# Kernel tuning notes

Measured on AMD Instinct MI355X. Metric: run time of the kernel, lower is better.

The kernel has to match this reference:

```python
import jax, jax.numpy as jnp
import numpy as np
from jax import lax

B, N, T_IN, F_IN = 64, 800, 15, 8
T_OUT = 12
H = 64
NC = 9
KS = [2, 2, 2, 3, 3, 3, 4, 4, 4]
DS = [1, 2, 4, 1, 2, 4, 1, 2, 4]


def setup_inputs() -> dict:
    key = jax.random.key(0)
    ks = jax.random.split(key, 16)
    s = 0.1
    f32 = jnp.float32
    inp = {}
    inp['A'] = jnp.zeros((1,), f32)  # deprecated graph arg, unused
    inp['X'] = jax.random.normal(ks[0], (B, N, T_IN, F_IN), f32)
    # dilated conv weights grouped by kernel size (comps 0-2 k=2, 3-5 k=3, 6-8 k=4)
    inp['convw2'] = jax.random.normal(ks[1], (3, F_IN, F_IN, 2), f32) * s
    inp['convw3'] = jax.random.normal(ks[2], (3, F_IN, F_IN, 3), f32) * s
    inp['convw4'] = jax.random.normal(ks[3], (3, F_IN, F_IN, 4), f32) * s
    inp['convb'] = jax.random.normal(ks[4], (NC, F_IN), f32) * s
    # encoder GRU params (PyTorch layout: W_ih (3H,F), W_hh (3H,H))
    inp['enc_wih'] = jax.random.normal(ks[5], (NC, 3 * H, F_IN), f32) * s
    inp['enc_whh'] = jax.random.normal(ks[6], (NC, 3 * H, H), f32) * s
    inp['enc_bih'] = jax.random.normal(ks[7], (NC, 3 * H), f32) * s
    inp['enc_bhh'] = jax.random.normal(ks[8], (NC, 3 * H), f32) * s
    # decoder GRUCell params (input size 1)
    inp['dec_wih'] = jax.random.normal(ks[9], (NC, 3 * H, 1), f32) * s
    inp['dec_whh'] = jax.random.normal(ks[10], (NC, 3 * H, H), f32) * s
    inp['dec_bih'] = jax.random.normal(ks[11], (NC, 3 * H), f32) * s
    inp['dec_bhh'] = jax.random.normal(ks[12], (NC, 3 * H), f32) * s
    # per-comp readout Linear(H, 1)
    inp['lin_w'] = jax.random.normal(ks[13], (NC, 1, H), f32) * s
    inp['lin_b'] = jax.random.normal(ks[14], (NC, 1), f32) * s
    # node-wise component mixing embedding
    inp['embed'] = jax.random.normal(ks[15], (N, NC), f32)
    return inp


def gru_cell(x, h, wih, whh, bih, bhh):
    # PyTorch GRU semantics
    gi = x @ wih.T + bih  # (B, 3H)
    gh = h @ whh.T + bhh  # (B, 3H)
    ir, iz, in_ = jnp.split(gi, 3, axis=-1)
    hr, hz, hn = jnp.split(gh, 3, axis=-1)
    r = jax.nn.sigmoid(ir + hr)
    z = jax.nn.sigmoid(iz + hz)
    n = jnp.tanh(in_ + r * hn)
    return (1.0 - z) * n + z * h


def reference(A, X, convw2, convw3, convw4, convb, enc_wih, enc_whh, enc_bih,
              enc_bhh, dec_wih, dec_whh, dec_bih, dec_bhh, lin_w, lin_b, embed):
    del A  # deprecated in pure TS model
    Xf = X.reshape(-1, T_IN, F_IN)            # (B*N, T, F)
    xt = jnp.transpose(Xf, (0, 2, 1))         # (B*N, F, T) for conv NCH
    last0 = Xf[:, -1, 0:1]                    # X1[-1, :, 0] -> (B*N, 1)
    BN = Xf.shape[0]
    conv_ws = [convw2[0], convw2[1], convw2[2], convw3[0], convw3[1],
               convw3[2], convw4[0], convw4[1], convw4[2]]
    outs = []
    for r in range(NC):
        # dilated conv over time, VALID padding (length shrinks by d*(k-1))
        h = lax.conv_general_dilated(xt, conv_ws[r], (1,), 'VALID',
                                     rhs_dilation=(DS[r],),
                                     dimension_numbers=('NCH', 'OIH', 'NCH'))
        h = h + convb[r][None, :, None]
        seq = jnp.transpose(h, (2, 0, 1))     # time-major (L, B*N, F)

        ewih, ewhh, ebih, ebhh = enc_wih[r], enc_whh[r], enc_bih[r], enc_bhh[r]

        def enc_step(hc, x_t):
            return gru_cell(x_t, hc, ewih, ewhh, ebih, ebhh), None

        h_enc, _ = lax.scan(enc_step, jnp.zeros((BN, H), X.dtype), seq)

        dwih, dwhh, dbih, dbhh = dec_wih[r], dec_whh[r], dec_bih[r], dec_bhh[r]
        lw, lb = lin_w[r], lin_b[r]

        def dec_step(carry, _):
            hd, lv = carry
            hd = gru_cell(lv, hd, dwih, dwhh, dbih, dbhh)
            v = hd @ lw.T + lb                # (B*N, 1)
            # torch code feeds value.detach() back in
            return (hd, lax.stop_gradient(v)), v[:, 0]

        _, vals = lax.scan(dec_step, (h_enc, last0), None, length=T_OUT)
        outs.append(jnp.transpose(vals).reshape(B, N, T_OUT))  # (B, N, T_out)
    out = jnp.stack(outs, axis=-1)            # (B, N, T_out, NC)
    w = jax.nn.softmax(embed, axis=-1)        # (N, NC)
    return jnp.einsum('bntc,nc->bnt', out, w)
```

## Files before the change

kernel.cpp:

```cpp
#include <hip/hip_runtime.h>
#include <hip/hip_bf16.h>
#include <stdint.h>

typedef unsigned short u16;
typedef unsigned int   u32;
typedef float f32x4  __attribute__((ext_vector_type(4)));
typedef short bf16x8 __attribute__((ext_vector_type(8)));

#define NSEQ 800
#define TOUT 12
#define NC   9
#define LOG2E  1.44269504088896340736f
#define LOG2E2 2.88539008177792681472f

#define BH_OFF 0
#define BX_OFF 24576
#define H_OFF  36864
#define LDS_TOTAL 53248

__device__ __forceinline__ u16 f2bf(float f){ union{float f;u32 i;}v; v.f=f; u32 x=v.i; return (u16)((x + 0x7fffu + ((x>>16)&1u))>>16); }
__device__ __forceinline__ u32 pkbf(float a, float b){
  union{ __hip_bfloat162 h2; u32 u; } v;
  v.h2 = __float22bfloat162_rn(float2{a,b});
  return v.u;
}

union BXU { uint4 u; bf16x8 v; };

__global__ __launch_bounds__(512, 2) void rnn_kernel(
  const float* __restrict__ X,
  const float* __restrict__ cw2, const float* __restrict__ cw3, const float* __restrict__ cw4,
  const float* __restrict__ cbv,
  const float* __restrict__ Ewih, const float* __restrict__ Ewhh,
  const float* __restrict__ Ebih, const float* __restrict__ Ebhh,
  const float* __restrict__ Dwih, const float* __restrict__ Dwhh,
  const float* __restrict__ Dbih, const float* __restrict__ Dbhh,
  const float* __restrict__ Lw,   const float* __restrict__ Lb,
  const float* __restrict__ emb,
  float* __restrict__ out)
{
  __shared__ char LDSC[LDS_TOTAL];
  const int tid = threadIdx.x;
  const int wv  = tid >> 6;
  const int l   = tid & 63;
  const int q   = l >> 4;
  const int n   = l & 15;
  const int r   = blockIdx.y;
  const int seqb = blockIdx.x*128 + wv*16;

  const int Kc[NC]={2,2,2,3,3,3,4,4,4};
  const int Dc[NC]={1,2,4,1,2,4,1,2,4};
  const int K = Kc[r], D = Dc[r];
  const int L = 15 - (K-1)*D;

  const int HB = H_OFF + wv*2048;
  *(uint4*)(LDSC + HB + l*32)      = uint4{0,0,0,0};
  *(uint4*)(LDSC + HB + l*32 + 16) = uint4{0,0,0,0};

  auto stage_Bh = [&](const float* __restrict__ whh){
    #pragma unroll 1
    for (int it=0; it<3; it++){
      int slot = it*512 + tid;
      int g = slot >> 6, fl = slot & 63;
      int ks = g/12, nt = g%12;
      int col = nt*16 + (fl&15);
      float s = (nt<8) ? LOG2E : LOG2E2;
      u32 w[4] = {0,0,0,0};
      #pragma unroll
      for (int j=0;j<8;j++){
        int hid = ((j&3)<<4) | (ks*8 + (fl>>4)*2 + (j>>2));
        w[j>>1] |= (u32)f2bf(s * whh[col*64 + hid]) << ((j&1)*16);
      }
      *(uint4*)(LDSC + BH_OFF + slot*16) = uint4{w[0],w[1],w[2],w[3]};
    }
  };
  auto stage_Bx_enc = [&](){
    const float* wih = Ewih + r*192*8;
    const float* cw  = (r<3) ? (cw2 + r*128) : (r<6) ? (cw3 + (r-3)*192) : (cw4 + (r-6)*256);
    #pragma unroll 1
    for (int it=0; it<2; it++){
      int slot = it*512 + tid;
      if (slot < 768){
        int g = slot >> 6, fl = slot & 63;
        int col = g*16 + (fl&15);
        int tap = fl>>4;
        float s = (g<8) ? LOG2E : LOG2E2;
        u32 w[4] = {0,0,0,0};
        if (tap < K){
          #pragma unroll
          for (int j=0;j<8;j++){
            float a = 0.f;
            #pragma unroll
            for (int o=0;o<8;o++) a += wih[col*8+o]*cw[(o*8+j)*K + tap];
            w[j>>1] |= (u32)f2bf(s*a) << ((j&1)*16);
          }
        }
        *(uint4*)(LDSC + BX_OFF + slot*16) = uint4{w[0],w[1],w[2],w[3]};
      }
    }
  };
  auto stage_Bx_dec = [&](){
    const float* dwih = Dwih + r*192;
    #pragma unroll 1
    for (int it=0; it<2; it++){
      int slot = it*512 + tid;
      if (slot < 768){
        int g = slot >> 6, fl = slot & 63;
        int col = g*16 + (fl&15);
        float s = (g<8) ? LOG2E : LOG2E2;
        u32 w0 = ((fl>>4)==0) ? (u32)f2bf(s*dwih[col]) : 0u;
        *(uint4*)(LDSC + BX_OFF + slot*16) = uint4{w0,0,0,0};
      }
    }
  };

  stage_Bh(Ewhh + (size_t)r*192*64);
  stage_Bx_enc();

  float bR4[4], bZ4[4], bNi4[4], bNh4[4];
  {
    const float* bi = Ebih + r*192; const float* bh2 = Ebhh + r*192;
    const float* wih = Ewih + r*192*8; const float* cb = cbv + r*8;
    #pragma unroll
    for (int ht=0; ht<4; ht++){
      int hid = ht*16 + n;
      float cR=0.f,cZ=0.f,cN=0.f;
      #pragma unroll
      for (int o=0;o<8;o++){
        cR += wih[hid*8+o]*cb[o];
        cZ += wih[(64+hid)*8+o]*cb[o];
        cN += wih[(128+hid)*8+o]*cb[o];
      }
      bR4[ht]  = LOG2E  * (bi[hid]     + bh2[hid]     + cR);
      bZ4[ht]  = LOG2E  * (bi[64+hid]  + bh2[64+hid]  + cZ);
      bNi4[ht] = LOG2E2 * (bi[128+hid]                + cN);
      bNh4[ht] = LOG2E2 *                bh2[128+hid];
    }
  }

  float hO[4][4];
  #pragma unroll
  for (int ht=0;ht<4;ht++) for (int i=0;i<4;i++) hO[ht][i]=0.f;

  const int ra0 = HB + n*128 + (((  q + n)&7)<<4);
  const int ra1 = HB + n*128 + (((4+q + n)&7)<<4);
  int wa[4];
  #pragma unroll
  for (int i=0;i<4;i++){
    int seq = q*4+i;
    wa[i] = HB + seq*128 + ((((n>>1) + seq)&7)<<4) + ((n&1)<<3);
  }

  auto step_core = [&](bf16x8 ax){
    bf16x8 a0 = *(const bf16x8*)(LDSC + ra0);
    bf16x8 a1 = *(const bf16x8*)(LDSC + ra1);
    float hsv[4]; u32 pk01[4], pk23[4];
    #pragma unroll
    for (int ht=0; ht<4; ht++){
      bf16x8 bR0 = *(const bf16x8*)(LDSC + BH_OFF + ((      ht)*64 + l)*16);
      bf16x8 bR1 = *(const bf16x8*)(LDSC + BH_OFF + ((12  + ht)*64 + l)*16);
      bf16x8 bZ0 = *(const bf16x8*)(LDSC + BH_OFF + (( 4 + ht)*64 + l)*16);
      bf16x8 bZ1 = *(const bf16x8*)(LDSC + BH_OFF + ((16  + ht)*64 + l)*16);
      bf16x8 bN0 = *(const bf16x8*)(LDSC + BH_OFF + (( 8 + ht)*64 + l)*16);
      bf16x8 bN1 = *(const bf16x8*)(LDSC + BH_OFF + ((20  + ht)*64 + l)*16);
      bf16x8 xR  = *(const bf16x8*)(LDSC + BX_OFF + ((      ht)*64 + l)*16);
      bf16x8 xZ  = *(const bf16x8*)(LDSC + BX_OFF + (( 4 + ht)*64 + l)*16);
      bf16x8 xN  = *(const bf16x8*)(LDSC + BX_OFF + (( 8 + ht)*64 + l)*16);
      f32x4 aR  = f32x4{bR4[ht],bR4[ht],bR4[ht],bR4[ht]};
      f32x4 aZ  = f32x4{bZ4[ht],bZ4[ht],bZ4[ht],bZ4[ht]};
      f32x4 aNi = f32x4{bNi4[ht],bNi4[ht],bNi4[ht],bNi4[ht]};
      f32x4 aNh = f32x4{bNh4[ht],bNh4[ht],bNh4[ht],bNh4[ht]};
      aR = __builtin_amdgcn_mfma_f32_16x16x32_bf16(a0, bR0, aR,0,0,0);
      aR = __builtin_amdgcn_mfma_f32_16x16x32_bf16(a1, bR1, aR,0,0,0);
      aR = __builtin_amdgcn_mfma_f32_16x16x32_bf16(ax, xR,  aR,0,0,0);
      aZ = __builtin_amdgcn_mfma_f32_16x16x32_bf16(a0, bZ0, aZ,0,0,0);
      aZ = __builtin_amdgcn_mfma_f32_16x16x32_bf16(a1, bZ1, aZ,0,0,0);
      aZ = __builtin_amdgcn_mfma_f32_16x16x32_bf16(ax, xZ,  aZ,0,0,0);
      aNh= __builtin_amdgcn_mfma_f32_16x16x32_bf16(a0, bN0, aNh,0,0,0);
      aNh= __builtin_amdgcn_mfma_f32_16x16x32_bf16(a1, bN1, aNh,0,0,0);
      aNi= __builtin_amdgcn_mfma_f32_16x16x32_bf16(ax, xN,  aNi,0,0,0);
      #pragma unroll
      for (int i=0;i<4;i++){
        float rr = __builtin_amdgcn_rcpf(1.f + __builtin_amdgcn_exp2f(-aR[i]));
        float zz = __builtin_amdgcn_rcpf(1.f + __builtin_amdgcn_exp2f(-aZ[i]));
        float y  = aNi[i] + rr*aNh[i];
        float nn = 1.f - 2.f*__builtin_amdgcn_rcpf(__builtin_amdgcn_exp2f(y) + 1.f);
        float hn = nn + zz*(hO[ht][i]-nn);
        hO[ht][i] = hn;
        if (ht==0)      hsv[i] = hn;
        else if (ht==1) pk01[i] = pkbf(hsv[i], hn);
        else if (ht==2) hsv[i] = hn;
        else            pk23[i] = pkbf(hsv[i], hn);
      }
    }
    #pragma unroll
    for (int i=0;i<4;i++){
      uint2 wv2; wv2.x = pk01[i]; wv2.y = pk23[i];
      *(uint2*)(LDSC + wa[i]) = wv2;
    }
  };

  const float* xb = X + (size_t)(seqb + n)*120 + ((q<K)? q:0)*D*8;
  float4 c0 = *(const float4*)(xb);
  float4 c1 = *(const float4*)(xb + 4);
  __syncthreads();
  #pragma unroll 1
  for (int t=0; t<L; t++){
    int tn = (t+1 < L) ? (t+1) : t;
    float4 n0 = *(const float4*)(xb + tn*8);
    float4 n1 = *(const float4*)(xb + tn*8 + 4);
    BXU a;
    a.u.x = __builtin_amdgcn_perm(__float_as_uint(c0.y), __float_as_uint(c0.x), 0x07060302u);
    a.u.y = __builtin_amdgcn_perm(__float_as_uint(c0.w), __float_as_uint(c0.z), 0x07060302u);
    a.u.z = __builtin_amdgcn_perm(__float_as_uint(c1.y), __float_as_uint(c1.x), 0x07060302u);
    a.u.w = __builtin_amdgcn_perm(__float_as_uint(c1.w), __float_as_uint(c1.z), 0x07060302u);
    step_core(a.v);
    c0 = n0; c1 = n1;
  }

  __syncthreads();
  stage_Bh(Dwhh + (size_t)r*192*64);
  stage_Bx_dec();
  {
    const float* bi = Dbih + r*192; const float* bh2 = Dbhh + r*192;
    #pragma unroll
    for (int ht=0; ht<4; ht++){
      int hid = ht*16 + n;
      bR4[ht]  = LOG2E  * (bi[hid]     + bh2[hid]);
      bZ4[ht]  = LOG2E  * (bi[64+hid]  + bh2[64+hid]);
      bNi4[ht] = LOG2E2 *  bi[128+hid];
      bNh4[ht] = LOG2E2 *  bh2[128+hid];
    }
  }
  float lwr[4];
  #pragma unroll
  for (int ht=0; ht<4; ht++) lwr[ht] = Lw[r*64 + ht*16 + n];
  const float lb_ = Lb[r];
  float wgt;
  {
    int nb = (seqb + n) % NSEQ;
    float e[NC], mx = -1e30f;
    #pragma unroll
    for (int c=0;c<NC;c++){ e[c] = emb[nb*NC+c]; mx = fmaxf(mx, e[c]); }
    float sm = 0.f;
    #pragma unroll
    for (int c=0;c<NC;c++) sm += __expf(e[c]-mx);
    wgt = __expf(e[r]-mx) / sm;
  }
  float lv = X[(size_t)(seqb + n)*120 + 112];
  __syncthreads();

  #pragma unroll 1
  for (int t=0; t<TOUT; t++){
    BXU a; a.u = uint4{0,0,0,0};
    if (q==0) a.u.x = (u32)f2bf(lv);
    step_core(a.v);
    float p[4];
    #pragma unroll
    for (int i=0;i<4;i++)
      p[i] = hO[0][i]*lwr[0] + hO[1][i]*lwr[1] + hO[2][i]*lwr[2] + hO[3][i]*lwr[3];
    #pragma unroll
    for (int m=1; m<16; m<<=1){
      #pragma unroll
      for (int i=0;i<4;i++) p[i] += __shfl_xor(p[i], m, 64);
    }
    float s0 = (n&2) ? p[2] : p[0];
    float s1 = (n&2) ? p[3] : p[1];
    float se = (n&1) ? s1 : s0;
    float v = __shfl(se, (n>>2)*16 + (n&3), 64) + lb_;
    lv = v;
    if (q==0) atomicAdd(out + (size_t)(seqb+n)*TOUT + t, wgt*v);
  }
}

extern "C" void kernel_launch(void* const* d_in, const int* in_sizes, int n_in,
                              void* d_out, int out_size, void* d_ws, size_t ws_size,
                              hipStream_t stream)
{
  float* out = (float*)d_out;
  hipMemsetAsync(out, 0, (size_t)out_size*sizeof(float), stream);

  dim3 g(NSEQ*64/128, NC);
  rnn_kernel<<<g, 512, 0, stream>>>(
    (const float*)d_in[1],
    (const float*)d_in[2], (const float*)d_in[3], (const float*)d_in[4],
    (const float*)d_in[5],
    (const float*)d_in[6], (const float*)d_in[7], (const float*)d_in[8], (const float*)d_in[9],
    (const float*)d_in[10],(const float*)d_in[11],(const float*)d_in[12],(const float*)d_in[13],
    (const float*)d_in[14],(const float*)d_in[15],
    (const float*)d_in[16],
    out);
}
```

Before: 924.1 us.

## Keep GRU hidden state in registers by transposing MFMA operand roles

Swaps the MFMA A/B operands so the weights act as the row operand and the hidden state as the column operand. The new hidden state then stays in each lane's registers in the layout the next step's MFMA needs. This removes the per-step LDS write/read round trip of the hidden state and its swizzle, and shrinks LDS usage. The weight staging permutation and bias vectors are re-laid out to match, and the readout reduction becomes a per-lane dot product plus two cross-lane shuffles. Launch bounds drop to one block per SIMD pair hint, which may change register allocation and occupancy.

```diff
diff --git a/kernel.cpp b/kernel.cpp
--- a/kernel.cpp
+++ b/kernel.cpp
@@ -15,8 +15,7 @@
 
 #define BH_OFF 0
 #define BX_OFF 24576
-#define H_OFF  36864
-#define LDS_TOTAL 53248
+#define LDS_TOTAL 36864
 
 __device__ __forceinline__ u16 f2bf(float f){ union{float f;u32 i;}v; v.f=f; u32 x=v.i; return (u16)((x + 0x7fffu + ((x>>16)&1u))>>16); }
 __device__ __forceinline__ u32 pkbf(float a, float b){
@@ -26,8 +25,9 @@
 }
 
 union BXU { uint4 u; bf16x8 v; };
-
-__global__ __launch_bounds__(512, 2) void rnn_kernel(
+union PKU { u32 w[4]; bf16x8 v; };
+
+__global__ __launch_bounds__(512, 1) void rnn_kernel(
   const float* __restrict__ X,
   const float* __restrict__ cw2, const float* __restrict__ cw3, const float* __restrict__ cw4,
   const float* __restrict__ cbv,
@@ -53,10 +53,6 @@
   const int K = Kc[r], D = Dc[r];
   const int L = 15 - (K-1)*D;
 
-  const int HB = H_OFF + wv*2048;
-  *(uint4*)(LDSC + HB + l*32)      = uint4{0,0,0,0};
-  *(uint4*)(LDSC + HB + l*32 + 16) = uint4{0,0,0,0};
-
   auto stage_Bh = [&](const float* __restrict__ whh){
     #pragma unroll 1
     for (int it=0; it<3; it++){
@@ -68,7 +64,7 @@
       u32 w[4] = {0,0,0,0};
       #pragma unroll
       for (int j=0;j<8;j++){
-        int hid = ((j&3)<<4) | (ks*8 + (fl>>4)*2 + (j>>2));
+        int hid = ((j&3)<<4) | ((fl>>4)<<2) | (ks<<1) | (j>>2);
         w[j>>1] |= (u32)f2bf(s * whh[col*64 + hid]) << ((j&1)*16);
       }
       *(uint4*)(LDSC + BH_OFF + slot*16) = uint4{w[0],w[1],w[2],w[3]};
@@ -117,88 +113,77 @@
   stage_Bh(Ewhh + (size_t)r*192*64);
   stage_Bx_enc();
 
-  float bR4[4], bZ4[4], bNi4[4], bNh4[4];
+  f32x4 bRq[4], bZq[4], bNiq[4], bNhq[4];
   {
     const float* bi = Ebih + r*192; const float* bh2 = Ebhh + r*192;
     const float* wih = Ewih + r*192*8; const float* cb = cbv + r*8;
     #pragma unroll
     for (int ht=0; ht<4; ht++){
-      int hid = ht*16 + n;
-      float cR=0.f,cZ=0.f,cN=0.f;
-      #pragma unroll
-      for (int o=0;o<8;o++){
-        cR += wih[hid*8+o]*cb[o];
-        cZ += wih[(64+hid)*8+o]*cb[o];
-        cN += wih[(128+hid)*8+o]*cb[o];
-      }
-      bR4[ht]  = LOG2E  * (bi[hid]     + bh2[hid]     + cR);
-      bZ4[ht]  = LOG2E  * (bi[64+hid]  + bh2[64+hid]  + cZ);
-      bNi4[ht] = LOG2E2 * (bi[128+hid]                + cN);
-      bNh4[ht] = LOG2E2 *                bh2[128+hid];
+      #pragma unroll
+      for (int rg=0; rg<4; rg++){
+        int hid = ht*16 + q*4 + rg;
+        float cR=0.f,cZ=0.f,cN=0.f;
+        #pragma unroll
+        for (int o=0;o<8;o++){
+          cR += wih[hid*8+o]*cb[o];
+          cZ += wih[(64+hid)*8+o]*cb[o];
+          cN += wih[(128+hid)*8+o]*cb[o];
+        }
+        bRq[ht][rg]  = LOG2E  * (bi[hid]     + bh2[hid]     + cR);
+        bZq[ht][rg]  = LOG2E  * (bi[64+hid]  + bh2[64+hid]  + cZ);
+        bNiq[ht][rg] = LOG2E2 * (bi[128+hid]                + cN);
+        bNhq[ht][rg] = LOG2E2 *                bh2[128+hid];
+      }
     }
   }
 
   float hO[4][4];
   #pragma unroll
   for (int ht=0;ht<4;ht++) for (int i=0;i<4;i++) hO[ht][i]=0.f;
-
-  const int ra0 = HB + n*128 + (((  q + n)&7)<<4);
-  const int ra1 = HB + n*128 + (((4+q + n)&7)<<4);
-  int wa[4];
-  #pragma unroll
-  for (int i=0;i<4;i++){
-    int seq = q*4+i;
-    wa[i] = HB + seq*128 + ((((n>>1) + seq)&7)<<4) + ((n&1)<<3);
-  }
-
-  auto step_core = [&](bf16x8 ax){
-    bf16x8 a0 = *(const bf16x8*)(LDSC + ra0);
-    bf16x8 a1 = *(const bf16x8*)(LDSC + ra1);
-    float hsv[4]; u32 pk01[4], pk23[4];
-    #pragma unroll
-    for (int ht=0; ht<4; ht++){
-      bf16x8 bR0 = *(const bf16x8*)(LDSC + BH_OFF + ((      ht)*64 + l)*16);
-      bf16x8 bR1 = *(const bf16x8*)(LDSC + BH_OFF + ((12  + ht)*64 + l)*16);
-      bf16x8 bZ0 = *(const bf16x8*)(LDSC + BH_OFF + (( 4 + ht)*64 + l)*16);
-      bf16x8 bZ1 = *(const bf16x8*)(LDSC + BH_OFF + ((16  + ht)*64 + l)*16);
-      bf16x8 bN0 = *(const bf16x8*)(LDSC + BH_OFF + (( 8 + ht)*64 + l)*16);
-      bf16x8 bN1 = *(const bf16x8*)(LDSC + BH_OFF + ((20  + ht)*64 + l)*16);
-      bf16x8 xR  = *(const bf16x8*)(LDSC + BX_OFF + ((      ht)*64 + l)*16);
-      bf16x8 xZ  = *(const bf16x8*)(LDSC + BX_OFF + (( 4 + ht)*64 + l)*16);
-      bf16x8 xN  = *(const bf16x8*)(LDSC + BX_OFF + (( 8 + ht)*64 + l)*16);
-      f32x4 aR  = f32x4{bR4[ht],bR4[ht],bR4[ht],bR4[ht]};
-      f32x4 aZ  = f32x4{bZ4[ht],bZ4[ht],bZ4[ht],bZ4[ht]};
-      f32x4 aNi = f32x4{bNi4[ht],bNi4[ht],bNi4[ht],bNi4[ht]};
-      f32x4 aNh = f32x4{bNh4[ht],bNh4[ht],bNh4[ht],bNh4[ht]};
-      aR = __builtin_amdgcn_mfma_f32_16x16x32_bf16(a0, bR0, aR,0,0,0);
-      aR = __builtin_amdgcn_mfma_f32_16x16x32_bf16(a1, bR1, aR,0,0,0);
-      aR = __builtin_amdgcn_mfma_f32_16x16x32_bf16(ax, xR,  aR,0,0,0);
-      aZ = __builtin_amdgcn_mfma_f32_16x16x32_bf16(a0, bZ0, aZ,0,0,0);
-      aZ = __builtin_amdgcn_mfma_f32_16x16x32_bf16(a1, bZ1, aZ,0,0,0);
-      aZ = __builtin_amdgcn_mfma_f32_16x16x32_bf16(ax, xZ,  aZ,0,0,0);
-      aNh= __builtin_amdgcn_mfma_f32_16x16x32_bf16(a0, bN0, aNh,0,0,0);
-      aNh= __builtin_amdgcn_mfma_f32_16x16x32_bf16(a1, bN1, aNh,0,0,0);
-      aNi= __builtin_amdgcn_mfma_f32_16x16x32_bf16(ax, xN,  aNi,0,0,0);
-      #pragma unroll
-      for (int i=0;i<4;i++){
-        float rr = __builtin_amdgcn_rcpf(1.f + __builtin_amdgcn_exp2f(-aR[i]));
-        float zz = __builtin_amdgcn_rcpf(1.f + __builtin_amdgcn_exp2f(-aZ[i]));
-        float y  = aNi[i] + rr*aNh[i];
-        float nn = 1.f - 2.f*__builtin_amdgcn_rcpf(__builtin_amdgcn_exp2f(y) + 1.f);
-        float hn = nn + zz*(hO[ht][i]-nn);
-        hO[ht][i] = hn;
-        if (ht==0)      hsv[i] = hn;
-        else if (ht==1) pk01[i] = pkbf(hsv[i], hn);
-        else if (ht==2) hsv[i] = hn;
-        else            pk23[i] = pkbf(hsv[i], hn);
-      }
-    }
-    #pragma unroll
-    for (int i=0;i<4;i++){
-      uint2 wv2; wv2.x = pk01[i]; wv2.y = pk23[i];
-      *(uint2*)(LDSC + wa[i]) = wv2;
-    }
-  };
+  PKU hp0, hp1;
+  hp0.w[0]=0;hp0.w[1]=0;hp0.w[2]=0;hp0.w[3]=0;
+  hp1.w[0]=0;hp1.w[1]=0;hp1.w[2]=0;hp1.w[3]=0;
+
+#define STEP_CORE(AX) do{ \
+    bf16x8 ax_ = (AX); \
+    _Pragma("unroll") \
+    for (int ht=0; ht<4; ht++){ \
+      bf16x8 bR0 = *(const bf16x8*)(LDSC + BH_OFF + ((      ht)*64 + l)*16); \
+      bf16x8 bR1 = *(const bf16x8*)(LDSC + BH_OFF + ((12  + ht)*64 + l)*16); \
+      bf16x8 bZ0 = *(const bf16x8*)(LDSC + BH_OFF + (( 4 + ht)*64 + l)*16); \
+      bf16x8 bZ1 = *(const bf16x8*)(LDSC + BH_OFF + ((16  + ht)*64 + l)*16); \
+      bf16x8 bN0 = *(const bf16x8*)(LDSC + BH_OFF + (( 8 + ht)*64 + l)*16); \
+      bf16x8 bN1 = *(const bf16x8*)(LDSC + BH_OFF + ((20  + ht)*64 + l)*16); \
+      bf16x8 xR  = *(const bf16x8*)(LDSC + BX_OFF + ((      ht)*64 + l)*16); \
+      bf16x8 xZ  = *(const bf16x8*)(LDSC + BX_OFF + (( 4 + ht)*64 + l)*16); \
+      bf16x8 xN  = *(const bf16x8*)(LDSC + BX_OFF + (( 8 + ht)*64 + l)*16); \
+      f32x4 aR  = bRq[ht]; \
+      f32x4 aZ  = bZq[ht]; \
+      f32x4 aNi = bNiq[ht]; \
+      f32x4 aNh = bNhq[ht]; \
+      aR = __builtin_amdgcn_mfma_f32_16x16x32_bf16(bR0, hp0.v, aR,0,0,0); \
+      aR = __builtin_amdgcn_mfma_f32_16x16x32_bf16(bR1, hp1.v, aR,0,0,0); \
+      aR = __builtin_amdgcn_mfma_f32_16x16x32_bf16(xR,  ax_,   aR,0,0,0); \
+      aZ = __builtin_amdgcn_mfma_f32_16x16x32_bf16(bZ0, hp0.v, aZ,0,0,0); \
+      aZ = __builtin_amdgcn_mfma_f32_16x16x32_bf16(bZ1, hp1.v, aZ,0,0,0); \
+      aZ = __builtin_amdgcn_mfma_f32_16x16x32_bf16(xZ,  ax_,   aZ,0,0,0); \
+      aNh= __builtin_amdgcn_mfma_f32_16x16x32_bf16(bN0, hp0.v, aNh,0,0,0); \
+      aNh= __builtin_amdgcn_mfma_f32_16x16x32_bf16(bN1, hp1.v, aNh,0,0,0); \
+      aNi= __builtin_amdgcn_mfma_f32_16x16x32_bf16(xN,  ax_,   aNi,0,0,0); \
+      _Pragma("unroll") \
+      for (int i=0;i<4;i++){ \
+        float rr = __builtin_amdgcn_rcpf(1.f + __builtin_amdgcn_exp2f(-aR[i])); \
+        float zz = __builtin_amdgcn_rcpf(1.f + __builtin_amdgcn_exp2f(-aZ[i])); \
+        float y  = aNi[i] + rr*aNh[i]; \
+        float nn = 1.f - 2.f*__builtin_amdgcn_rcpf(__builtin_amdgcn_exp2f(y) + 1.f); \
+        hO[ht][i] = nn + zz*(hO[ht][i]-nn); \
+      } \
+    } \
+    hp0.w[0]=pkbf(hO[0][0],hO[1][0]); hp0.w[1]=pkbf(hO[2][0],hO[3][0]); \
+    hp0.w[2]=pkbf(hO[0][1],hO[1][1]); hp0.w[3]=pkbf(hO[2][1],hO[3][1]); \
+    hp1.w[0]=pkbf(hO[0][2],hO[1][2]); hp1.w[1]=pkbf(hO[2][2],hO[3][2]); \
+    hp1.w[2]=pkbf(hO[0][3],hO[1][3]); hp1.w[3]=pkbf(hO[2][3],hO[3][3]); \
+  }while(0)
 
   const float* xb = X + (size_t)(seqb + n)*120 + ((q<K)? q:0)*D*8;
   float4 c0 = *(const float4*)(xb);
@@ -214,7 +199,7 @@
     a.u.y = __builtin_amdgcn_perm(__float_as_uint(c0.w), __float_as_uint(c0.z), 0x07060302u);
     a.u.z = __builtin_amdgcn_perm(__float_as_uint(c1.y), __float_as_uint(c1.x), 0x07060302u);
     a.u.w = __builtin_amdgcn_perm(__float_as_uint(c1.w), __float_as_uint(c1.z), 0x07060302u);
-    step_core(a.v);
+    STEP_CORE(a.v);
     c0 = n0; c1 = n1;
   }
 
@@ -225,16 +210,22 @@
     const float* bi = Dbih + r*192; const float* bh2 = Dbhh + r*192;
     #pragma unroll
     for (int ht=0; ht<4; ht++){
-      int hid = ht*16 + n;
-      bR4[ht]  = LOG2E  * (bi[hid]     + bh2[hid]);
-      bZ4[ht]  = LOG2E  * (bi[64+hid]  + bh2[64+hid]);
-      bNi4[ht] = LOG2E2 *  bi[128+hid];
-      bNh4[ht] = LOG2E2 *  bh2[128+hid];
-    }
-  }
-  float lwr[4];
+      #pragma unroll
+      for (int rg=0; rg<4; rg++){
+        int hid = ht*16 + q*4 + rg;
+        bRq[ht][rg]  = LOG2E  * (bi[hid]     + bh2[hid]);
+        bZq[ht][rg]  = LOG2E  * (bi[64+hid]  + bh2[64+hid]);
+        bNiq[ht][rg] = LOG2E2 *  bi[128+hid];
+        bNhq[ht][rg] = LOG2E2 *  bh2[128+hid];
+      }
+    }
+  }
+  f32x4 lwA[4];
   #pragma unroll
-  for (int ht=0; ht<4; ht++) lwr[ht] = Lw[r*64 + ht*16 + n];
+  for (int ht=0; ht<4; ht++)
+    #pragma unroll
+    for (int rg=0; rg<4; rg++)
+      lwA[ht][rg] = Lw[r*64 + ht*16 + q*4 + rg];
   const float lb_ = Lb[r];
   float wgt;
   {
@@ -254,20 +245,16 @@
   for (int t=0; t<TOUT; t++){
     BXU a; a.u = uint4{0,0,0,0};
     if (q==0) a.u.x = (u32)f2bf(lv);
-    step_core(a.v);
-    float p[4];
-    #pragma unroll
-    for (int i=0;i<4;i++)
-      p[i] = hO[0][i]*lwr[0] + hO[1][i]*lwr[1] + hO[2][i]*lwr[2] + hO[3][i]*lwr[3];
-    #pragma unroll
-    for (int m=1; m<16; m<<=1){
-      #pragma unroll
-      for (int i=0;i<4;i++) p[i] += __shfl_xor(p[i], m, 64);
-    }
-    float s0 = (n&2) ? p[2] : p[0];
-    float s1 = (n&2) ? p[3] : p[1];
-    float se = (n&1) ? s1 : s0;
-    float v = __shfl(se, (n>>2)*16 + (n&3), 64) + lb_;
+    STEP_CORE(a.v);
+    float p = 0.f;
+    #pragma unroll
+    for (int ht=0; ht<4; ht++)
+      #pragma unroll
+      for (int i=0;i<4;i++)
+        p += hO[ht][i]*lwA[ht][i];
+    p += __shfl_xor(p, 16, 64);
+    p += __shfl_xor(p, 32, 64);
+    float v = p + lb_;
     lv = v;
     if (q==0) atomicAdd(out + (size_t)(seqb+n)*TOUT + t, wgt*v);
   }
```

Result: slower. 1.204 ms (+30.2%).

## Precompute bf16 weight images in a prep kernel and keep both in LDS

Applied to the files above, without the earlier changes.

Adds a small prep kernel that, once per component, builds the bf16 MFMA weight images for encoder and decoder, the folded conv-into-input-projection weights, the bias vectors and the softmax mixing weights, and writes them to workspace. The main kernel now only copies a contiguous image into LDS and reads the biases and weights. This removes the repeated per-block weight conversion, the conv folding and the mid-kernel restaging with its barrier. The cost is that shared memory per block grows from about 53 KB to about 90 KB, which may cut resident blocks per CU below the two requested by the launch bounds, and there is an extra kernel launch.

```diff
diff --git a/kernel.cpp b/kernel.cpp
--- a/kernel.cpp
+++ b/kernel.cpp
@@ -13,10 +13,16 @@
 #define LOG2E  1.44269504088896340736f
 #define LOG2E2 2.88539008177792681472f
 
-#define BH_OFF 0
-#define BX_OFF 24576
-#define H_OFF  36864
-#define LDS_TOTAL 53248
+#define WIMG_STRIDE 73728
+#define LDS_BHE 0
+#define LDS_BXE 24576
+#define LDS_BHD 36864
+#define LDS_BXD 61440
+#define LDS_H   73728
+#define LDS_TOTAL 90112
+#define BIASE_OFF 663552
+#define BIASD_OFF 672768
+#define WGT_OFF   681984
 
 __device__ __forceinline__ u16 f2bf(float f){ union{float f;u32 i;}v; v.f=f; u32 x=v.i; return (u16)((x + 0x7fffu + ((x>>16)&1u))>>16); }
 __device__ __forceinline__ u32 pkbf(float a, float b){
@@ -27,16 +33,116 @@
 
 union BXU { uint4 u; bf16x8 v; };
 
-__global__ __launch_bounds__(512, 2) void rnn_kernel(
-  const float* __restrict__ X,
+__global__ void prep_kernel(
   const float* __restrict__ cw2, const float* __restrict__ cw3, const float* __restrict__ cw4,
   const float* __restrict__ cbv,
   const float* __restrict__ Ewih, const float* __restrict__ Ewhh,
   const float* __restrict__ Ebih, const float* __restrict__ Ebhh,
   const float* __restrict__ Dwih, const float* __restrict__ Dwhh,
   const float* __restrict__ Dbih, const float* __restrict__ Dbhh,
-  const float* __restrict__ Lw,   const float* __restrict__ Lb,
   const float* __restrict__ emb,
+  char* __restrict__ ws)
+{
+  const int r = blockIdx.x;
+  const int tid = threadIdx.x;
+  const int K = (r<3) ? 2 : ((r<6) ? 3 : 4);
+  char* wimg = ws + (size_t)r*WIMG_STRIDE;
+
+  const float* ewhh = Ewhh + (size_t)r*192*64;
+  const float* dwhh = Dwhh + (size_t)r*192*64;
+  #pragma unroll 1
+  for (int s = tid; s < 1536; s += 512){
+    int g = s >> 6, fl = s & 63;
+    int ks = g/12, nt = g%12;
+    int col = nt*16 + (fl&15);
+    float sc = (nt<8) ? LOG2E : LOG2E2;
+    u32 we[4] = {0,0,0,0}, wd[4] = {0,0,0,0};
+    #pragma unroll
+    for (int j=0;j<8;j++){
+      int hid = ((j&3)<<4) | (ks*8 + (fl>>4)*2 + (j>>2));
+      we[j>>1] |= (u32)f2bf(sc * ewhh[col*64 + hid]) << ((j&1)*16);
+      wd[j>>1] |= (u32)f2bf(sc * dwhh[col*64 + hid]) << ((j&1)*16);
+    }
+    *(uint4*)(wimg + LDS_BHE + s*16) = uint4{we[0],we[1],we[2],we[3]};
+    *(uint4*)(wimg + LDS_BHD + s*16) = uint4{wd[0],wd[1],wd[2],wd[3]};
+  }
+  const float* wih = Ewih + r*192*8;
+  const float* cw  = (r<3) ? (cw2 + r*128) : (r<6) ? (cw3 + (r-3)*192) : (cw4 + (r-6)*256);
+  const float* dwih = Dwih + r*192;
+  #pragma unroll 1
+  for (int s = tid; s < 768; s += 512){
+    int g = s >> 6, fl = s & 63;
+    int col = g*16 + (fl&15);
+    int tap = fl>>4;
+    float sc = (g<8) ? LOG2E : LOG2E2;
+    u32 w[4] = {0,0,0,0};
+    if (tap < K){
+      #pragma unroll
+      for (int j=0;j<8;j++){
+        float a = 0.f;
+        #pragma unroll
+        for (int o=0;o<8;o++) a += wih[col*8+o]*cw[(o*8+j)*K + tap];
+        w[j>>1] |= (u32)f2bf(sc*a) << ((j&1)*16);
+      }
+    }
+    *(uint4*)(wimg + LDS_BXE + s*16) = uint4{w[0],w[1],w[2],w[3]};
+    u32 w0 = (tap==0) ? (u32)f2bf(sc*dwih[col]) : 0u;
+    *(uint4*)(wimg + LDS_BXD + s*16) = uint4{w0,0,0,0};
+  }
+  if (tid < 16){
+    int n = tid;
+    const float* bi = Ebih + r*192; const float* bh2 = Ebhh + r*192;
+    const float* cb = cbv + r*8;
+    float* be = (float*)(ws + BIASE_OFF) + ((size_t)r*16 + n)*16;
+    #pragma unroll
+    for (int ht=0; ht<4; ht++){
+      int hid = ht*16 + n;
+      float cR=0.f,cZ=0.f,cN=0.f;
+      #pragma unroll
+      for (int o=0;o<8;o++){
+        cR += wih[hid*8+o]*cb[o];
+        cZ += wih[(64+hid)*8+o]*cb[o];
+        cN += wih[(128+hid)*8+o]*cb[o];
+      }
+      be[ht]    = LOG2E  * (bi[hid]     + bh2[hid]     + cR);
+      be[4+ht]  = LOG2E  * (bi[64+hid]  + bh2[64+hid]  + cZ);
+      be[8+ht]  = LOG2E2 * (bi[128+hid]                + cN);
+      be[12+ht] = LOG2E2 *                bh2[128+hid];
+    }
+  } else if (tid < 32){
+    int n = tid - 16;
+    const float* bi = Dbih + r*192; const float* bh2 = Dbhh + r*192;
+    float* bd = (float*)(ws + BIASD_OFF) + ((size_t)r*16 + n)*16;
+    #pragma unroll
+    for (int ht=0; ht<4; ht++){
+      int hid = ht*16 + n;
+      bd[ht]    = LOG2E  * (bi[hid]     + bh2[hid]);
+      bd[4+ht]  = LOG2E  * (bi[64+hid]  + bh2[64+hid]);
+      bd[8+ht]  = LOG2E2 *  bi[128+hid];
+      bd[12+ht] = LOG2E2 *  bh2[128+hid];
+    }
+  }
+  if (r == 0){
+    float* wg = (float*)(ws + WGT_OFF);
+    #pragma unroll 1
+    for (int nb = tid; nb < NSEQ; nb += 512){
+      float e[NC], mx = -1e30f;
+      #pragma unroll
+      for (int c=0;c<NC;c++){ e[c] = emb[nb*NC+c]; mx = fmaxf(mx, e[c]); }
+      float sm = 0.f;
+      #pragma unroll
+      for (int c=0;c<NC;c++){ e[c] = __expf(e[c]-mx); sm += e[c]; }
+      float inv = 1.f/sm;
+      #pragma unroll
+      for (int c=0;c<NC;c++) wg[nb*NC+c] = e[c]*inv;
+    }
+  }
+}
+
+__global__ __launch_bounds__(512, 2) void rnn_kernel(
+  const float* __restrict__ X,
+  const float* __restrict__ Lw, const float* __restrict__ Lb,
+  const char* __restrict__ ws,
   float* __restrict__ out)
 {
   __shared__ char LDSC[LDS_TOTAL];
@@ -53,89 +159,30 @@
   const int K = Kc[r], D = Dc[r];
   const int L = 15 - (K-1)*D;
 
-  const int HB = H_OFF + wv*2048;
+  const int HB = LDS_H + wv*2048;
   *(uint4*)(LDSC + HB + l*32)      = uint4{0,0,0,0};
   *(uint4*)(LDSC + HB + l*32 + 16) = uint4{0,0,0,0};
 
-  auto stage_Bh = [&](const float* __restrict__ whh){
+  {
+    const uint4* src = (const uint4*)(ws + (size_t)r*WIMG_STRIDE);
     #pragma unroll 1
-    for (int it=0; it<3; it++){
-      int slot = it*512 + tid;
-      int g = slot >> 6, fl = slot & 63;
-      int ks = g/12, nt = g%12;
-      int col = nt*16 + (fl&15);
-      float s = (nt<8) ? LOG2E : LOG2E2;
-      u32 w[4] = {0,0,0,0};
-      #pragma unroll
-      for (int j=0;j<8;j++){
-        int hid = ((j&3)<<4) | (ks*8 + (fl>>4)*2 + (j>>2));
-        w[j>>1] |= (u32)f2bf(s * whh[col*64 + hid]) << ((j&1)*16);
-      }
-      *(uint4*)(LDSC + BH_OFF + slot*16) = uint4{w[0],w[1],w[2],w[3]};
-    }
-  };
-  auto stage_Bx_enc = [&](){
-    const float* wih = Ewih + r*192*8;
-    const float* cw  = (r<3) ? (cw2 + r*128) : (r<6) ? (cw3 + (r-3)*192) : (cw4 + (r-6)*256);
-    #pragma unroll 1
-    for (int it=0; it<2; it++){
-      int slot = it*512 + tid;
-      if (slot < 768){
-        int g = slot >> 6, fl = slot & 63;
-        int col = g*16 + (fl&15);
-        int tap = fl>>4;
-        float s = (g<8) ? LOG2E : LOG2E2;
-        u32 w[4] = {0,0,0,0};
-        if (tap < K){
-          #pragma unroll
-          for (int j=0;j<8;j++){
-            float a = 0.f;
-            #pragma unroll
-            for (int o=0;o<8;o++) a += wih[col*8+o]*cw[(o*8+j)*K + tap];
-            w[j>>1] |= (u32)f2bf(s*a) << ((j&1)*16);
-          }
-        }
-        *(uint4*)(LDSC + BX_OFF + slot*16) = uint4{w[0],w[1],w[2],w[3]};
-      }
-    }
-  };
-  auto stage_Bx_dec = [&](){
-    const float* dwih = Dwih + r*192;
-    #pragma unroll 1
-    for (int it=0; it<2; it++){
-      int slot = it*512 + tid;
-      if (slot < 768){
-        int g = slot >> 6, fl = slot & 63;
-        int col = g*16 + (fl&15);
-        float s = (g<8) ? LOG2E : LOG2E2;
-        u32 w0 = ((fl>>4)==0) ? (u32)f2bf(s*dwih[col]) : 0u;
-        *(uint4*)(LDSC + BX_OFF + slot*16) = uint4{w0,0,0,0};
-      }
-    }
-  };
-
-  stage_Bh(Ewhh + (size_t)r*192*64);
-  stage_Bx_enc();
+    for (int it=0; it<9; it++){
+      int idx = it*512 + tid;
+      *(uint4*)(LDSC + idx*16) = src[idx];
+    }
+  }
 
   float bR4[4], bZ4[4], bNi4[4], bNh4[4];
   {
-    const float* bi = Ebih + r*192; const float* bh2 = Ebhh + r*192;
-    const float* wih = Ewih + r*192*8; const float* cb = cbv + r*8;
-    #pragma unroll
-    for (int ht=0; ht<4; ht++){
-      int hid = ht*16 + n;
-      float cR=0.f,cZ=0.f,cN=0.f;
-      #pragma unroll
-      for (int o=0;o<8;o++){
-        cR += wih[hid*8+o]*cb[o];
-        cZ += wih[(64+hid)*8+o]*cb[o];
-        cN += wih[(128+hid)*8+o]*cb[o];
-      }
-      bR4[ht]  = LOG2E  * (bi[hid]     + bh2[hid]     + cR);
-      bZ4[ht]  = LOG2E  * (bi[64+hid]  + bh2[64+hid]  + cZ);
-      bNi4[ht] = LOG2E2 * (bi[128+hid]                + cN);
-      bNh4[ht] = LOG2E2 *                bh2[128+hid];
-    }
+    const float* be = (const float*)(ws + BIASE_OFF) + ((size_t)r*16 + n)*16;
+    float4 v0 = *(const float4*)(be);
+    float4 v1 = *(const float4*)(be+4);
+    float4 v2 = *(const float4*)(be+8);
+    float4 v3 = *(const float4*)(be+12);
+    bR4[0]=v0.x; bR4[1]=v0.y; bR4[2]=v0.z; bR4[3]=v0.w;
+    bZ4[0]=v1.x; bZ4[1]=v1.y; bZ4[2]=v1.z; bZ4[3]=v1.w;
+    bNi4[0]=v2.x; bNi4[1]=v2.y; bNi4[2]=v2.z; bNi4[3]=v2.w;
+    bNh4[0]=v3.x; bNh4[1]=v3.y; bNh4[2]=v3.z; bNh4[3]=v3.w;
   }
 
   float hO[4][4];
@@ -151,21 +198,21 @@
     wa[i] = HB + seq*128 + ((((n>>1) + seq)&7)<<4) + ((n&1)<<3);
   }
 
-  auto step_core = [&](bf16x8 ax){
+  auto step_core = [&](int bho, int bxo, bf16x8 ax){
     bf16x8 a0 = *(const bf16x8*)(LDSC + ra0);
     bf16x8 a1 = *(const bf16x8*)(LDSC + ra1);
     float hsv[4]; u32 pk01[4], pk23[4];
     #pragma unroll
     for (int ht=0; ht<4; ht++){
-      bf16x8 bR0 = *(const bf16x8*)(LDSC + BH_OFF + ((      ht)*64 + l)*16);
-      bf16x8 bR1 = *(const bf16x8*)(LDSC + BH_OFF + ((12  + ht)*64 + l)*16);
-      bf16x8 bZ0 = *(const bf16x8*)(LDSC + BH_OFF + (( 4 + ht)*64 + l)*16);
-      bf16x8 bZ1 = *(const bf16x8*)(LDSC + BH_OFF + ((16  + ht)*64 + l)*16);
-      bf16x8 bN0 = *(const bf16x8*)(LDSC + BH_OFF + (( 8 + ht)*64 + l)*16);
-      bf16x8 bN1 = *(const bf16x8*)(LDSC + BH_OFF + ((20  + ht)*64 + l)*16);
-      bf16x8 xR  = *(const bf16x8*)(LDSC + BX_OFF + ((      ht)*64 + l)*16);
-      bf16x8 xZ  = *(const bf16x8*)(LDSC + BX_OFF + (( 4 + ht)*64 + l)*16);
-      bf16x8 xN  = *(const bf16x8*)(LDSC + BX_OFF + (( 8 + ht)*64 + l)*16);
+      bf16x8 bR0 = *(const bf16x8*)(LDSC + bho + ((      ht)*64 + l)*16);
+      bf16x8 bR1 = *(const bf16x8*)(LDSC + bho + ((12  + ht)*64 + l)*16);
+      bf16x8 bZ0 = *(const bf16x8*)(LDSC + bho + (( 4 + ht)*64 + l)*16);
+      bf16x8 bZ1 = *(const bf16x8*)(LDSC + bho + ((16  + ht)*64 + l)*16);
+      bf16x8 bN0 = *(const bf16x8*)(LDSC + bho + (( 8 + ht)*64 + l)*16);
+      bf16x8 bN1 = *(const bf16x8*)(LDSC + bho + ((20  + ht)*64 + l)*16);
+      bf16x8 xR  = *(const bf16x8*)(LDSC + bxo + ((      ht)*64 + l)*16);
+      bf16x8 xZ  = *(const bf16x8*)(LDSC + bxo + (( 4 + ht)*64 + l)*16);
+      bf16x8 xN  = *(const bf16x8*)(LDSC + bxo + (( 8 + ht)*64 + l)*16);
       f32x4 aR  = f32x4{bR4[ht],bR4[ht],bR4[ht],bR4[ht]};
       f32x4 aZ  = f32x4{bZ4[ht],bZ4[ht],bZ4[ht],bZ4[ht]};
       f32x4 aNi = f32x4{bNi4[ht],bNi4[ht],bNi4[ht],bNi4[ht]};
@@ -214,47 +261,33 @@
     a.u.y = __builtin_amdgcn_perm(__float_as_uint(c0.w), __float_as_uint(c0.z), 0x07060302u);
     a.u.z = __builtin_amdgcn_perm(__float_as_uint(c1.y), __float_as_uint(c1.x), 0x07060302u);
     a.u.w = __builtin_amdgcn_perm(__float_as_uint(c1.w), __float_as_uint(c1.z), 0x07060302u);
-    step_core(a.v);
+    step_core(LDS_BHE, LDS_BXE, a.v);
     c0 = n0; c1 = n1;
   }
 
-  __syncthreads();
-  stage_Bh(Dwhh + (size_t)r*192*64);
-  stage_Bx_dec();
   {
-    const float* bi = Dbih + r*192; const float* bh2 = Dbhh + r*192;
-    #pragma unroll
-    for (int ht=0; ht<4; ht++){
-      int hid = ht*16 + n;
-      bR4[ht]  = LOG2E  * (bi[hid]     + bh2[hid]);
-      bZ4[ht]  = LOG2E  * (bi[64+hid]  + bh2[64+hid]);
-      bNi4[ht] = LOG2E2 *  bi[128+hid];
-      bNh4[ht] = LOG2E2 *  bh2[128+hid];
-    }
+    const float* bd = (const float*)(ws + BIASD_OFF) + ((size_t)r*16 + n)*16;
+    float4 v0 = *(const float4*)(bd);
+    float4 v1 = *(const float4*)(bd+4);
+    float4 v2 = *(const float4*)(bd+8);
+    float4 v3 = *(const float4*)(bd+12);
+    bR4[0]=v0.x; bR4[1]=v0.y; bR4[2]=v0.z; bR4[3]=v0.w;
+    bZ4[0]=v1.x; bZ4[1]=v1.y; bZ4[2]=v1.z; bZ4[3]=v1.w;
+    bNi4[0]=v2.x; bNi4[1]=v2.y; bNi4[2]=v2.z; bNi4[3]=v2.w;
+    bNh4[0]=v3.x; bNh4[1]=v3.y; bNh4[2]=v3.z; bNh4[3]=v3.w;
   }
   float lwr[4];
   #pragma unroll
   for (int ht=0; ht<4; ht++) lwr[ht] = Lw[r*64 + ht*16 + n];
   const float lb_ = Lb[r];
-  float wgt;
-  {
-    int nb = (seqb + n) % NSEQ;
-    float e[NC], mx = -1e30f;
-    #pragma unroll
-    for (int c=0;c<NC;c++){ e[c] = emb[nb*NC+c]; mx = fmaxf(mx, e[c]); }
-    float sm = 0.f;
-    #pragma unroll
-    for (int c=0;c<NC;c++) sm += __expf(e[c]-mx);
-    wgt = __expf(e[r]-mx) / sm;
-  }
+  const float wgt = ((const float*)(ws + WGT_OFF))[((seqb + n) % NSEQ)*NC + r];
   float lv = X[(size_t)(seqb + n)*120 + 112];
-  __syncthreads();
 
   #pragma unroll 1
   for (int t=0; t<TOUT; t++){
     BXU a; a.u = uint4{0,0,0,0};
     if (q==0) a.u.x = (u32)f2bf(lv);
-    step_core(a.v);
+    step_core(LDS_BHD, LDS_BXD, a.v);
     float p[4];
     #pragma unroll
     for (int i=0;i<4;i++)
@@ -280,14 +313,18 @@
   float* out = (float*)d_out;
   hipMemsetAsync(out, 0, (size_t)out_size*sizeof(float), stream);
 
-  dim3 g(NSEQ*64/128, NC);
-  rnn_kernel<<<g, 512, 0, stream>>>(
-    (const float*)d_in[1],
+  prep_kernel<<<dim3(NC), 512, 0, stream>>>(
     (const float*)d_in[2], (const float*)d_in[3], (const float*)d_in[4],
     (const float*)d_in[5],
     (const float*)d_in[6], (const float*)d_in[7], (const float*)d_in[8], (const float*)d_in[9],
     (const float*)d_in[10],(const float*)d_in[11],(const float*)d_in[12],(const float*)d_in[13],
-    (const float*)d_in[14],(const float*)d_in[15],
     (const float*)d_in[16],
+    (char*)d_ws);
+
+  dim3 g(NSEQ*64/128, NC);
+  rnn_kernel<<<g, 512, 0, stream>>>(
+    (const float*)d_in[1],
+    (const float*)d_in[14], (const float*)d_in[15],
+    (const char*)d_ws,
     out);
 }
```

Result: faster. 757.7 us (-18.0%).
